# Kernel tuning notes

Hardware: AMD Instinct MI355X
Metric: run time of the kernel (lower is better)

## Reference

```python
import jax, jax.numpy as jnp
import numpy as np

NH = 8          # attention heads
TOP_K = 2       # MoE top-k


def _ln(x, g, b, eps=1e-5):
    mu = x.mean(-1, keepdims=True)
    var = ((x - mu) ** 2).mean(-1, keepdims=True)
    return (x - mu) * jax.lax.rsqrt(var + eps) * g + b


def setup_inputs() -> dict:
    key = jax.random.key(0)
    ks = jax.random.split(key, 12)
    B, C, S, P, E, HID, NEXP, NCLS = 128, 3, 224, 16, 256, 1024, 6, 1000
    N = (S // P) ** 2
    def n(k, shape, scale=0.02):
        return scale * jax.random.normal(k, shape, jnp.float32)
    return dict(
        x=jax.random.normal(ks[0], (B, C, S, S), jnp.float32),
        conv_w=n(ks[1], (E, C, P, P)),
        conv_b=jnp.zeros((E,), jnp.float32),
        pos_embed=n(ks[2], (1, N, E)),
        ln1_g=jnp.ones((E,), jnp.float32), ln1_b=jnp.zeros((E,), jnp.float32),
        wqkv=n(ks[3], (3 * E, E)), bqkv=jnp.zeros((3 * E,), jnp.float32),
        wo=n(ks[4], (E, E)), bo=jnp.zeros((E,), jnp.float32),
        router_w=n(ks[5], (NEXP, E)), router_b=jnp.zeros((NEXP,), jnp.float32),
        w1=n(ks[6], (NEXP, E, HID)), b1=jnp.zeros((NEXP, HID), jnp.float32),
        w2=n(ks[7], (NEXP, HID, E)), b2=jnp.zeros((NEXP, E), jnp.float32),
        ln2_g=jnp.ones((E,), jnp.float32), ln2_b=jnp.zeros((E,), jnp.float32),
        head_w=n(ks[8], (NCLS, E)), head_b=jnp.zeros((NCLS,), jnp.float32),
    )


def reference(x, conv_w, conv_b, pos_embed, ln1_g, ln1_b, wqkv, bqkv, wo, bo,
              router_w, router_b, w1, b1, w2, b2, ln2_g, ln2_b, head_w, head_b):
    B, C, S, _ = x.shape
    E, _, P, _ = conv_w.shape
    G = S // P
    N = G * G
    hd = E // NH
    # --- patch embedding: strided conv == per-patch linear ---
    xr = x.reshape(B, C, G, P, G, P)
    tok = jnp.einsum('bchpwq,ecpq->bhwe', xr, conv_w).reshape(B, N, E) + conv_b
    tok = tok + pos_embed  # dropout is identity in eval
    # --- self-attention block (pre-norm, residual) ---
    xn = _ln(tok, ln1_g, ln1_b)
    qkv = xn @ wqkv.T + bqkv
    q, k, v = jnp.split(qkv, 3, axis=-1)
    q = q.reshape(B, N, NH, hd)
    k = k.reshape(B, N, NH, hd)
    v = v.reshape(B, N, NH, hd)
    scores = jnp.einsum('bqhd,bkhd->bhqk', q, k) / np.float32(np.sqrt(hd))
    attn = jax.nn.softmax(scores, axis=-1)
    ao = jnp.einsum('bhqk,bkhd->bqhd', attn, v).reshape(B, N, E)
    x1 = tok + ao @ wo.T + bo
    # --- MoE (top-k routing, eval: no noise) ---
    T = B * N
    flat = x1.reshape(T, E)
    probs = jax.nn.softmax(flat @ router_w.T + router_b, axis=-1)
    topw, topi = jax.lax.top_k(probs, TOP_K)  # [T,k]
    out = jnp.zeros_like(flat)
    n_experts = router_w.shape[0]
    for e in range(n_experts):  # fixed small expert loop
        gate = jnp.sum(jnp.where(topi == e, topw, 0.0), axis=-1)  # [T], 0 if unrouted
        h = jax.nn.gelu(flat @ w1[e] + b1[e], approximate=False)
        y = h @ w2[e] + b2[e]
        out = out + gate[:, None] * y
    # --- final norm, pool, head ---
    x2 = _ln(out.reshape(B, N, E), ln2_g, ln2_b)
    pooled = x2.mean(axis=1)
    return pooled @ head_w.T + head_b
```

## Files before the change

### kernel.cpp

```cpp
#include <hip/hip_runtime.h>
#include <hip/hip_bf16.h>

typedef unsigned short u16;
typedef short short8 __attribute__((ext_vector_type(8)));
typedef float f32x4 __attribute__((ext_vector_type(4)));

#define T_TOK 25088
#define NTOK 196
#define SWZ(r, c) ((((((c) >> 3) ^ ((r) & 7)) << 3)) | ((c) & 7))

__device__ __forceinline__ u16 bfbits(float v) {
  __hip_bfloat16 h = __float2bfloat16(v);
  return *reinterpret_cast<u16*>(&h);
}
__device__ __forceinline__ float b2f(u16 u) {
  __hip_bfloat16 h = *reinterpret_cast<__hip_bfloat16*>(&u);
  return __bfloat162float(h);
}
__device__ __forceinline__ void fsplit(float v, u16& hi, u16& lo) {
  hi = bfbits(v);
  lo = bfbits(v - b2f(hi));
}

template<int EPI, bool SPLITA>
__global__ __launch_bounds__(256) void gemm_bs(
    const u16* __restrict__ A, const u16* __restrict__ Al,
    const u16* __restrict__ Bh, const u16* __restrict__ Bl,
    int M, int N, int K,
    const float* __restrict__ bias, const float* __restrict__ extra,
    float* __restrict__ outf, u16* __restrict__ obh)
{
  __shared__ u16 As[128][40];
  __shared__ u16 Asl[SPLITA ? 128 : 1][40];
  __shared__ u16 Bsh[128][40], Bsl[128][40];
  const int tid = threadIdx.x;
  const int lane = tid & 63, wave = tid >> 6;
  const int wm = wave >> 1, wn = wave & 1;
  const int row0 = blockIdx.x * 128, col0 = blockIdx.y * 128;

  const int r0 = tid >> 2, r1 = r0 + 64, co = (tid & 3) * 8;
  const int ar0 = row0 + r0, ar1 = row0 + r1;

  f32x4 acc[4][4];
  const f32x4 zero = {0.f, 0.f, 0.f, 0.f};
#pragma unroll
  for (int i = 0; i < 4; ++i)
#pragma unroll
    for (int j = 0; j < 4; ++j) acc[i][j] = zero;

  const int rsel = lane & 15, ksel = (lane >> 4) * 8;

  short8 ra0, ra1, rl0, rl1, rb0, rb1, rc0, rc1;
  auto issue = [&](int k0) {
    ra0 = *(const short8*)(A + (size_t)ar0 * K + k0 + co);
    ra1 = *(const short8*)(A + (size_t)ar1 * K + k0 + co);
    if constexpr (SPLITA) {
      rl0 = *(const short8*)(Al + (size_t)ar0 * K + k0 + co);
      rl1 = *(const short8*)(Al + (size_t)ar1 * K + k0 + co);
    }
    rb0 = *(const short8*)(Bh + (size_t)(col0 + r0) * K + k0 + co);
    rb1 = *(const short8*)(Bh + (size_t)(col0 + r1) * K + k0 + co);
    rc0 = *(const short8*)(Bl + (size_t)(col0 + r0) * K + k0 + co);
    rc1 = *(const short8*)(Bl + (size_t)(col0 + r1) * K + k0 + co);
  };
  auto commit = [&]() {
    *(short8*)&As[r0][co] = ra0;
    *(short8*)&As[r1][co] = ra1;
    if constexpr (SPLITA) {
      *(short8*)&Asl[r0][co] = rl0;
      *(short8*)&Asl[r1][co] = rl1;
    }
    *(short8*)&Bsh[r0][co] = rb0;
    *(short8*)&Bsh[r1][co] = rb1;
    *(short8*)&Bsl[r0][co] = rc0;
    *(short8*)&Bsl[r1][co] = rc1;
  };

  issue(0);
  commit();
  __syncthreads();

  for (int k0 = 0;;) {
    const bool more = (k0 + 32 < K);
    if (more) issue(k0 + 32);
    short8 af[4], al4[4], bh4[4], bl4[4];
#pragma unroll
    for (int i = 0; i < 4; ++i) {
      af[i] = *(const short8*)&As[wm * 64 + i * 16 + rsel][ksel];
      if constexpr (SPLITA) al4[i] = *(const short8*)&Asl[wm * 64 + i * 16 + rsel][ksel];
    }
#pragma unroll
    for (int j = 0; j < 4; ++j) {
      bh4[j] = *(const short8*)&Bsh[wn * 64 + j * 16 + rsel][ksel];
      bl4[j] = *(const short8*)&Bsl[wn * 64 + j * 16 + rsel][ksel];
    }
#pragma unroll
    for (int i = 0; i < 4; ++i)
#pragma unroll
      for (int j = 0; j < 4; ++j) {
        acc[i][j] = __builtin_amdgcn_mfma_f32_16x16x32_bf16(af[i], bh4[j], acc[i][j], 0, 0, 0);
        if constexpr (SPLITA)
          acc[i][j] = __builtin_amdgcn_mfma_f32_16x16x32_bf16(al4[i], bh4[j], acc[i][j], 0, 0, 0);
        acc[i][j] = __builtin_amdgcn_mfma_f32_16x16x32_bf16(af[i], bl4[j], acc[i][j], 0, 0, 0);
      }
    k0 += 32;
    if (!more) break;
    __syncthreads();
    commit();
    __syncthreads();
  }

#pragma unroll
  for (int i = 0; i < 4; ++i) {
#pragma unroll
    for (int j = 0; j < 4; ++j) {
#pragma unroll
      for (int r = 0; r < 4; ++r) {
        int grow = row0 + wm * 64 + i * 16 + (lane >> 4) * 4 + r;
        int gcol = col0 + wn * 64 + j * 16 + (lane & 15);
        float v = acc[i][j][r] + bias[gcol];
        size_t oi = (size_t)grow * N + gcol;
        if constexpr (EPI == 1) {
          v += extra[(size_t)(grow % NTOK) * N + gcol];
          outf[oi] = v;
        } else if constexpr (EPI == 2) {
          v += extra[oi];
          outf[oi] = v;
          obh[oi] = bfbits(v);
        } else if constexpr (EPI == 5) {
          obh[oi] = bfbits(v);
        }
      }
    }
  }
}

__global__ __launch_bounds__(512, 4) void moe_fused(
    const u16* __restrict__ x1h,
    const u16* __restrict__ w1, const u16* __restrict__ w2,
    const float* __restrict__ b1, const float* __restrict__ b2,
    const float* __restrict__ gates,
    const int* __restrict__ idx_all, const int* __restrict__ cnt_all,
    const int* __restrict__ base_all,
    float* __restrict__ yslot)
{
  const int e = blockIdx.z;
  const int Meff = cnt_all[e];
  const int row0 = blockIdx.x * 64;
  if (row0 >= Meff) return;
  const int* gidx = idx_all + (size_t)e * T_TOK;
  const int hbase = base_all[e];
  const u16* W1 = w1 + (size_t)e * 262144;
  const u16* W2 = w2 + (size_t)e * 262144;
  const float* B1 = b1 + e * 1024;
  const float* B2 = b2 + e * 256;

  __shared__ u16 Xs[64][256];
  __shared__ u16 Hs[64][128];
  __shared__ u16 Ws[2 * 128 * 64];

  const int tid = threadIdx.x, lane = tid & 63, wave = tid >> 6;
  const int wm = wave >> 2, wn = wave & 3;
  const int rsel = lane & 15, ksel = (lane >> 4) * 8;
  const f32x4 zero = {0.f, 0.f, 0.f, 0.f};

  const int w1r = tid >> 2, w1c = ((2 * tid) & 7) * 8;
  const int w2r = tid >> 1, w2c = ((4 * tid) & 7) * 8;

  short8 w1a = *(const short8*)(W1 + (size_t)w1r * 256 + w1c);
  short8 w1b = *(const short8*)(W1 + (size_t)w1r * 256 + w1c + 8);
  for (int ch = tid; ch < 2048; ch += 512) {
    int r = ch >> 5, c = (ch & 31) * 8;
    int ar = gidx[min(row0 + r, Meff - 1)];
    *(short8*)&Xs[r][SWZ(r, c)] = *(const short8*)(x1h + (size_t)ar * 256 + c);
  }

  f32x4 acc2[2][4];
#pragma unroll
  for (int i = 0; i < 2; ++i)
#pragma unroll
    for (int j = 0; j < 4; ++j) acc2[i][j] = zero;

  f32x4 acc1[2][2];

  auto ph1 = [&](int st, int buf) {
#pragma unroll
    for (int kk = 0; kk < 2; ++kk) {
      int ra0 = wm * 32 + rsel, ra1 = ra0 + 16;
      int kc = st * 64 + kk * 32 + ksel;
      short8 a0 = *(const short8*)&Xs[ra0][SWZ(ra0, kc)];
      short8 a1 = *(const short8*)&Xs[ra1][SWZ(ra1, kc)];
      int rb0 = wn * 32 + rsel, rb1 = rb0 + 16;
      int wc = kk * 32 + ksel;
      short8 b0 = *(const short8*)&Ws[buf * 8192 + rb0 * 64 + SWZ(rb0, wc)];
      short8 b1 = *(const short8*)&Ws[buf * 8192 + rb1 * 64 + SWZ(rb1, wc)];
      acc1[0][0] = __builtin_amdgcn_mfma_f32_16x16x32_bf16(a0, b0, acc1[0][0], 0, 0, 0);
      acc1[0][1] = __builtin_amdgcn_mfma_f32_16x16x32_bf16(a0, b1, acc1[0][1], 0, 0, 0);
      acc1[1][0] = __builtin_amdgcn_mfma_f32_16x16x32_bf16(a1, b0, acc1[1][0], 0, 0, 0);
      acc1[1][1] = __builtin_amdgcn_mfma_f32_16x16x32_bf16(a1, b1, acc1[1][1], 0, 0, 0);
    }
  };
  auto ph2 = [&](int st) {
#pragma unroll
    for (int kk = 0; kk < 2; ++kk) {
      int ra0 = wm * 32 + rsel, ra1 = ra0 + 16;
      int kc = st * 64 + kk * 32 + ksel;
      short8 a0 = *(const short8*)&Hs[ra0][SWZ(ra0, kc)];
      short8 a1 = *(const short8*)&Hs[ra1][SWZ(ra1, kc)];
      int wc = kk * 32 + ksel;
#pragma unroll
      for (int nj = 0; nj < 4; ++nj) {
        int nr = wn * 64 + nj * 16 + rsel;
        short8 b = *(const short8*)&Ws[nr * 64 + SWZ(nr, wc)];
        acc2[0][nj] = __builtin_amdgcn_mfma_f32_16x16x32_bf16(a0, b, acc2[0][nj], 0, 0, 0);
        acc2[1][nj] = __builtin_amdgcn_mfma_f32_16x16x32_bf16(a1, b, acc2[1][nj], 0, 0, 0);
      }
    }
  };

  for (int hc = 0; hc < 8; ++hc) {
    const u16* W1c = W1 + (size_t)hc * 128 * 256;
    const u16* W2c = W2 + hc * 128;
    short8 q0 = *(const short8*)(W2c + (size_t)w2r * 1024 + w2c);
    short8 q1 = *(const short8*)(W2c + (size_t)w2r * 1024 + w2c + 8);
    short8 q2 = *(const short8*)(W2c + (size_t)w2r * 1024 + w2c + 16);
    short8 q3 = *(const short8*)(W2c + (size_t)w2r * 1024 + w2c + 24);

#pragma unroll
    for (int i = 0; i < 2; ++i) {
      acc1[i][0] = zero; acc1[i][1] = zero;
    }

    *(short8*)&Ws[w1r * 64 + SWZ(w1r, w1c)] = w1a;
    *(short8*)&Ws[w1r * 64 + SWZ(w1r, w1c + 8)] = w1b;
    short8 p0 = *(const short8*)(W1c + (size_t)w1r * 256 + 64 + w1c);
    short8 p1 = *(const short8*)(W1c + (size_t)w1r * 256 + 64 + w1c + 8);
    __syncthreads();
    short8 r0 = *(const short8*)(W1c + (size_t)w1r * 256 + 128 + w1c);
    short8 r1 = *(const short8*)(W1c + (size_t)w1r * 256 + 128 + w1c + 8);
    ph1(0, 0);
    *(short8*)&Ws[8192 + w1r * 64 + SWZ(w1r, w1c)] = p0;
    *(short8*)&Ws[8192 + w1r * 64 + SWZ(w1r, w1c + 8)] = p1;
    __syncthreads();
    p0 = *(const short8*)(W1c + (size_t)w1r * 256 + 192 + w1c);
    p1 = *(const short8*)(W1c + (size_t)w1r * 256 + 192 + w1c + 8);
    ph1(1, 1);
    *(short8*)&Ws[w1r * 64 + SWZ(w1r, w1c)] = r0;
    *(short8*)&Ws[w1r * 64 + SWZ(w1r, w1c + 8)] = r1;
    __syncthreads();
    ph1(2, 0);
    *(short8*)&Ws[8192 + w1r * 64 + SWZ(w1r, w1c)] = p0;
    *(short8*)&Ws[8192 + w1r * 64 + SWZ(w1r, w1c + 8)] = p1;
    __syncthreads();
    ph1(3, 1);

#pragma unroll
    for (int mi = 0; mi < 2; ++mi)
#pragma unroll
      for (int nj = 0; nj < 2; ++nj)
#pragma unroll
        for (int r = 0; r < 4; ++r) {
          int tr = wm * 32 + mi * 16 + (lane >> 4) * 4 + r;
          int tc = wn * 32 + nj * 16 + rsel;
          float v = acc1[mi][nj][r] + B1[hc * 128 + tc];
          float u = 1.5957691216057308f * (v + 0.044715f * v * v * v);
          Hs[tr][SWZ(tr, tc)] = bfbits(v / (1.f + __expf(-u)));
        }
    __syncthreads();

    *(short8*)&Ws[w2r * 64 + SWZ(w2r, w2c)] = q0;
    *(short8*)&Ws[w2r * 64 + SWZ(w2r, w2c + 8)] = q1;
    *(short8*)&Ws[w2r * 64 + SWZ(w2r, w2c + 16)] = q2;
    *(short8*)&Ws[w2r * 64 + SWZ(w2r, w2c + 24)] = q3;
    q0 = *(const short8*)(W2c + (size_t)w2r * 1024 + 64 + w2c);
    q1 = *(const short8*)(W2c + (size_t)w2r * 1024 + 64 + w2c + 8);
    q2 = *(const short8*)(W2c + (size_t)w2r * 1024 + 64 + w2c + 16);
    q3 = *(const short8*)(W2c + (size_t)w2r * 1024 + 64 + w2c + 24);
    __syncthreads();
    ph2(0);
    __syncthreads();
    *(short8*)&Ws[w2r * 64 + SWZ(w2r, w2c)] = q0;
    *(short8*)&Ws[w2r * 64 + SWZ(w2r, w2c + 8)] = q1;
    *(short8*)&Ws[w2r * 64 + SWZ(w2r, w2c + 16)] = q2;
    *(short8*)&Ws[w2r * 64 + SWZ(w2r, w2c + 24)] = q3;
    if (hc < 7) {
      w1a = *(const short8*)(W1 + (size_t)((hc + 1) * 128 + w1r) * 256 + w1c);
      w1b = *(const short8*)(W1 + (size_t)((hc + 1) * 128 + w1r) * 256 + w1c + 8);
    }
    __syncthreads();
    ph2(1);
    __syncthreads();
  }

#pragma unroll
  for (int mi = 0; mi < 2; ++mi)
#pragma unroll
    for (int r = 0; r < 4; ++r) {
      int grow = row0 + wm * 32 + mi * 16 + (lane >> 4) * 4 + r;
      if (grow < Meff) {
        int tk = gidx[grow];
        float gt = gates[(size_t)tk * 6 + e];
#pragma unroll
        for (int nj = 0; nj < 4; ++nj) {
          int gcol = wn * 64 + nj * 16 + rsel;
          yslot[(size_t)(hbase + grow) * 256 + gcol] = gt * (acc2[mi][nj][r] + B2[gcol]);
        }
      }
    }
}

__global__ void im2col_split(const float* __restrict__ x,
                             u16* __restrict__ Aph, u16* __restrict__ Apl) {
  int id = blockIdx.x * 256 + threadIdx.x;
  if (id >= T_TOK * 192) return;
  int t = id / 192, kk = id - t * 192;
  int k4 = kk * 4;
  int c = k4 >> 8, rem = k4 & 255, p = rem >> 4, q = rem & 15;
  int b = t / 196, n = t - b * 196, gh = n / 14, gw = n - gh * 14;
  const float4 v = *(const float4*)(x + ((size_t)(b * 3 + c) * 224 + gh * 16 + p) * 224 + gw * 16 + q);
  u16 h0, l0, h1, l1, h2, l2, h3, l3;
  fsplit(v.x, h0, l0); fsplit(v.y, h1, l1); fsplit(v.z, h2, l2); fsplit(v.w, h3, l3);
  *(ushort4*)(Aph + (size_t)t * 768 + k4) = make_ushort4(h0, h1, h2, h3);
  *(ushort4*)(Apl + (size_t)t * 768 + k4) = make_ushort4(l0, l1, l2, l3);
}

__global__ __launch_bounds__(256) void ln_kernel(const float* __restrict__ in,
    const float* __restrict__ g, const float* __restrict__ b, u16* __restrict__ oh)
{
  const int lane = threadIdx.x & 63;
  const int t = blockIdx.x * 4 + (threadIdx.x >> 6);
  const float4 v = *(const float4*)(in + (size_t)t * 256 + lane * 4);
  float s = v.x + v.y + v.z + v.w;
  float sq = v.x * v.x + v.y * v.y + v.z * v.z + v.w * v.w;
#pragma unroll
  for (int o = 32; o >= 1; o >>= 1) {
    s  += __shfl_xor(s,  o, 64);
    sq += __shfl_xor(sq, o, 64);
  }
  float mu = s * (1.f / 256.f);
  float var = sq * (1.f / 256.f) - mu * mu;
  float rstd = rsqrtf(var + 1e-5f);
  const float4 gv = *(const float4*)(g + lane * 4);
  const float4 bv = *(const float4*)(b + lane * 4);
  *(ushort4*)(oh + (size_t)t * 256 + lane * 4) = make_ushort4(
      bfbits((v.x - mu) * rstd * gv.x + bv.x), bfbits((v.y - mu) * rstd * gv.y + bv.y),
      bfbits((v.z - mu) * rstd * gv.z + bv.z), bfbits((v.w - mu) * rstd * gv.w + bv.w));
}

__global__ __launch_bounds__(256) void ln2_combine(const float* __restrict__ yslot,
    const int* __restrict__ invslot,
    const float* __restrict__ g, const float* __restrict__ b, float* __restrict__ outf)
{
  const int lane = threadIdx.x & 63;
  const int t = blockIdx.x * 4 + (threadIdx.x >> 6);
  const int s0 = invslot[t * 2], s1 = invslot[t * 2 + 1];
  const float4 a = *(const float4*)(yslot + (size_t)s0 * 256 + lane * 4);
  const float4 c = *(const float4*)(yslot + (size_t)s1 * 256 + lane * 4);
  float4 v = make_float4(a.x + c.x, a.y + c.y, a.z + c.z, a.w + c.w);
  float s = v.x + v.y + v.z + v.w;
  float sq = v.x * v.x + v.y * v.y + v.z * v.z + v.w * v.w;
#pragma unroll
  for (int o = 32; o >= 1; o >>= 1) {
    s  += __shfl_xor(s,  o, 64);
    sq += __shfl_xor(sq, o, 64);
  }
  float mu = s * (1.f / 256.f);
  float var = sq * (1.f / 256.f) - mu * mu;
  float rstd = rsqrtf(var + 1e-5f);
  const float4 gv = *(const float4*)(g + lane * 4);
  const float4 bv = *(const float4*)(b + lane * 4);
  *(float4*)(outf + (size_t)t * 256 + lane * 4) = make_float4(
      (v.x - mu) * rstd * gv.x + bv.x, (v.y - mu) * rstd * gv.y + bv.y,
      (v.z - mu) * rstd * gv.z + bv.z, (v.w - mu) * rstd * gv.w + bv.w);
}

__global__ __launch_bounds__(256) void attn_mfma(const u16* __restrict__ qkvb,
                                                 u16* __restrict__ aoh, u16* __restrict__ aol) {
  __shared__ u16 Qs[208][40];
  __shared__ u16 Ks[208][40];
  __shared__ u16 Vt[32][256];
  __shared__ u16 Ps[4][16][232];
  const int tid = threadIdx.x, lane = tid & 63, wave = tid >> 6;
  const int b = blockIdx.x >> 3, h = blockIdx.x & 7;
  const size_t base = (size_t)b * 196 * 768 + h * 32;
  const short8 z8 = {0, 0, 0, 0, 0, 0, 0, 0};

  for (int idx = tid; idx < 832; idx += 256) {
    int r = idx >> 2, c = (idx & 3) * 8;
    short8 q = z8, k = z8;
    if (r < 196) {
      q = *(const short8*)(qkvb + base + (size_t)r * 768 + c);
// ... 193 lines not shown
  const int e = blockIdx.z;
  const int bc = blockIdx.x * 32, br = blockIdx.y * 32;
  const int tx = threadIdx.x & 31, ty = threadIdx.x >> 5;
  const float* src = in + (size_t)e * R * C;
#pragma unroll
  for (int i = 0; i < 32; i += 8)
    tile[ty + i][tx] = src[(size_t)(br + ty + i) * C + bc + tx];
  __syncthreads();
#pragma unroll
  for (int i = 0; i < 32; i += 8) {
    size_t di = (size_t)e * R * C + (size_t)(bc + ty + i) * R + br + tx;
    oh[di] = bfbits(tile[tx][ty + i]);
  }
}

extern "C" void kernel_launch(void* const* d_in, const int* in_sizes, int n_in,
                              void* d_out, int out_size, void* d_ws, size_t ws_size,
                              hipStream_t stream) {
  (void)in_sizes; (void)n_in; (void)out_size; (void)ws_size;
  const float* x      = (const float*)d_in[0];
  const float* conv_w = (const float*)d_in[1];
  const float* conv_b = (const float*)d_in[2];
  const float* pos    = (const float*)d_in[3];
  const float* ln1_g  = (const float*)d_in[4];
  const float* ln1_b  = (const float*)d_in[5];
  const float* wqkv   = (const float*)d_in[6];
  const float* bqkv   = (const float*)d_in[7];
  const float* wo     = (const float*)d_in[8];
  const float* bo     = (const float*)d_in[9];
  const float* rw     = (const float*)d_in[10];
  const float* rb     = (const float*)d_in[11];
  const float* w1     = (const float*)d_in[12];
  const float* b1     = (const float*)d_in[13];
  const float* w2     = (const float*)d_in[14];
  const float* b2     = (const float*)d_in[15];
  const float* ln2_g  = (const float*)d_in[16];
  const float* ln2_b  = (const float*)d_in[17];
  const float* hw     = (const float*)d_in[18];
  const float* hb     = (const float*)d_in[19];
  float* out = (float*)d_out;

  const int T = T_TOK;
  char* ws = (char*)d_ws;
  size_t off = 0;
  auto alloc = [&](size_t bytes) -> void* {
    void* p = ws + off;
    off += (bytes + 255) & ~(size_t)255;
    return p;
  };
  u16*   Aph    = (u16*)  alloc((size_t)T * 768 * 2);
  u16*   Apl    = (u16*)  alloc((size_t)T * 768 * 2);
  float* tok    = (float*)alloc((size_t)T * 256 * 4);
  u16*   xnh    = (u16*)  alloc((size_t)T * 256 * 2);
  u16*   qkvb   = (u16*)  alloc((size_t)T * 768 * 2);
  u16*   aoh    = (u16*)  alloc((size_t)T * 256 * 2);
  u16*   aol    = (u16*)  alloc((size_t)T * 256 * 2);
  float* x1f    = (float*)alloc((size_t)T * 256 * 4);
  u16*   x1h    = (u16*)  alloc((size_t)T * 256 * 2);
  float* gates  = (float*)alloc((size_t)T * 6 * 4);
  int*   idx    = (int*)  alloc((size_t)6 * T * 4);
  int*   cnt    = (int*)  alloc(256);
  int*   base   = (int*)  alloc(256);
  int*   nslot  = (int*)  alloc((size_t)T * 4);
  int*   invslot= (int*)  alloc((size_t)2 * T * 4);
  float* pooled = (float*)alloc((size_t)128 * 256 * 4);
  u16*   cwh    = (u16*)  alloc((size_t)196608 * 2);
  u16*   cwl    = (u16*)  alloc((size_t)196608 * 2);
  u16*   wqh    = (u16*)  alloc((size_t)196608 * 2);
  u16*   wql    = (u16*)  alloc((size_t)196608 * 2);
  u16*   woh    = (u16*)  alloc((size_t)65536 * 2);
  u16*   wol    = (u16*)  alloc((size_t)65536 * 2);
  u16*   w1th   = (u16*)  alloc((size_t)6 * 262144 * 2);
  u16*   w2th   = (u16*)  alloc((size_t)6 * 262144 * 2);
  float* yslot = (float*)aoh;
  float* x2    = (float*)ws;

  cast_split_kernel<<<192, 256, 0, stream>>>(conv_w, cwh, cwl, 49152);
  cast_split_kernel<<<192, 256, 0, stream>>>(wqkv, wqh, wql, 49152);
  cast_split_kernel<<<64, 256, 0, stream>>>(wo, woh, wol, 16384);
  transpose_cast<<<dim3(32, 8, 6), 256, 0, stream>>>(w1, w1th, 256, 1024);
  transpose_cast<<<dim3(8, 32, 6), 256, 0, stream>>>(w2, w2th, 1024, 256);

  im2col_split<<<18816, 256, 0, stream>>>(x, Aph, Apl);
  gemm_bs<1, true><<<dim3(196, 2), 256, 0, stream>>>(Aph, Apl, cwh, cwl, T, 256, 768,
      conv_b, pos, tok, nullptr);

  ln_kernel<<<6272, 256, 0, stream>>>(tok, ln1_g, ln1_b, xnh);
  gemm_bs<5, false><<<dim3(196, 6), 256, 0, stream>>>(xnh, nullptr, wqh, wql, T, 768, 256,
      bqkv, nullptr, nullptr, qkvb);
  attn_mfma<<<1024, 256, 0, stream>>>(qkvb, aoh, aol);
  gemm_bs<2, true><<<dim3(196, 2), 256, 0, stream>>>(aoh, aol, woh, wol, T, 256, 256,
      bo, tok, x1f, x1h);

  router_kernel<<<6272, 256, 0, stream>>>(x1f, rw, rb, gates);
  hipMemsetAsync(cnt, 0, 256, stream);
  scatter_kernel<<<98, 256, 0, stream>>>(gates, cnt, idx);
  prefix6_kernel<<<1, 64, 0, stream>>>(cnt, base);
  hipMemsetAsync(nslot, 0, (size_t)T * 4, stream);
  slotmap_kernel<<<dim3(98, 6), 256, 0, stream>>>(idx, cnt, base, nslot, invslot);
  moe_fused<<<dim3(392, 1, 6), 512, 0, stream>>>(x1h, w1th, w2th,
      b1, b2, gates, idx, cnt, base, yslot);

  ln2_combine<<<6272, 256, 0, stream>>>(yslot, invslot, ln2_g, ln2_b, x2);
  pool_kernel<<<128, 256, 0, stream>>>(x2, pooled);
  head_kernel<<<128, 256, 0, stream>>>(pooled, hw, hb, out);
}
```

Measured before the change: 429.2 us.

## Load GEMM B operands directly from global into registers and shrink tiles

Measured after the change: 471.7 us. +9.9%, slower.

```diff
diff --git a/kernel.cpp b/kernel.cpp
--- a/kernel.cpp
+++ b/kernel.cpp
@@ -23,101 +23,94 @@
 }
 
 template<int EPI, bool SPLITA>
-__global__ __launch_bounds__(256) void gemm_bs(
+__global__ __launch_bounds__(256, 4) void gemm_bs(
     const u16* __restrict__ A, const u16* __restrict__ Al,
     const u16* __restrict__ Bh, const u16* __restrict__ Bl,
     int M, int N, int K,
     const float* __restrict__ bias, const float* __restrict__ extra,
     float* __restrict__ outf, u16* __restrict__ obh)
 {
-  __shared__ u16 As[128][40];
-  __shared__ u16 Asl[SPLITA ? 128 : 1][40];
-  __shared__ u16 Bsh[128][40], Bsl[128][40];
+  __shared__ u16 As[2][64][40];
+  __shared__ u16 Asl[SPLITA ? 2 : 1][64][40];
   const int tid = threadIdx.x;
-  const int lane = tid & 63, wave = tid >> 6;
-  const int wm = wave >> 1, wn = wave & 1;
-  const int row0 = blockIdx.x * 128, col0 = blockIdx.y * 128;
-
-  const int r0 = tid >> 2, r1 = r0 + 64, co = (tid & 3) * 8;
-  const int ar0 = row0 + r0, ar1 = row0 + r1;
-
-  f32x4 acc[4][4];
+  const int lane = tid & 63, wn = tid >> 6;
+  const int row0 = blockIdx.x * 64, col0 = blockIdx.y * 128;
+  const int rsel = lane & 15, ksel = (lane >> 4) * 8;
+
+  const int sr = tid >> 2, sc = (tid & 3) * 8;
+  const int ar = row0 + sr;
+
+  const u16* bph0 = Bh + (size_t)(col0 + wn * 32 + rsel) * K;
+  const u16* bph1 = Bh + (size_t)(col0 + wn * 32 + 16 + rsel) * K;
+  const u16* bpl0 = Bl + (size_t)(col0 + wn * 32 + rsel) * K;
+  const u16* bpl1 = Bl + (size_t)(col0 + wn * 32 + 16 + rsel) * K;
+
+  f32x4 acc[4][2];
   const f32x4 zero = {0.f, 0.f, 0.f, 0.f};
 #pragma unroll
-  for (int i = 0; i < 4; ++i)
-#pragma unroll
-    for (int j = 0; j < 4; ++j) acc[i][j] = zero;
-
-  const int rsel = lane & 15, ksel = (lane >> 4) * 8;
-
-  short8 ra0, ra1, rl0, rl1, rb0, rb1, rc0, rc1;
-  auto issue = [&](int k0) {
-    ra0 = *(const short8*)(A + (size_t)ar0 * K + k0 + co);
-    ra1 = *(const short8*)(A + (size_t)ar1 * K + k0 + co);
-    if constexpr (SPLITA) {
-      rl0 = *(const short8*)(Al + (size_t)ar0 * K + k0 + co);
-      rl1 = *(const short8*)(Al + (size_t)ar1 * K + k0 + co);
-    }
-    rb0 = *(const short8*)(Bh + (size_t)(col0 + r0) * K + k0 + co);
-    rb1 = *(const short8*)(Bh + (size_t)(col0 + r1) * K + k0 + co);
-    rc0 = *(const short8*)(Bl + (size_t)(col0 + r0) * K + k0 + co);
-    rc1 = *(const short8*)(Bl + (size_t)(col0 + r1) * K + k0 + co);
+  for (int i = 0; i < 4; ++i) { acc[i][0] = zero; acc[i][1] = zero; }
+
+  short8 ra, rl;
+  auto issueA = [&](int k0) {
+    ra = *(const short8*)(A + (size_t)ar * K + k0 + sc);
+    if constexpr (SPLITA) rl = *(const short8*)(Al + (size_t)ar * K + k0 + sc);
   };
-  auto commit = [&]() {
-    *(short8*)&As[r0][co] = ra0;
-    *(short8*)&As[r1][co] = ra1;
-    if constexpr (SPLITA) {
-      *(short8*)&Asl[r0][co] = rl0;
-      *(short8*)&Asl[r1][co] = rl1;
-    }
-    *(short8*)&Bsh[r0][co] = rb0;
-    *(short8*)&Bsh[r1][co] = rb1;
-    *(short8*)&Bsl[r0][co] = rc0;
-    *(short8*)&Bsl[r1][co] = rc1;
+  auto commitA = [&](int buf) {
+    *(short8*)&As[buf][sr][sc] = ra;
+    if constexpr (SPLITA) *(short8*)&Asl[buf][sr][sc] = rl;
   };
 
-  issue(0);
-  commit();
-  __syncthreads();
-
+  issueA(0);
+  commitA(0);
+  short8 b0 = *(const short8*)(bph0 + ksel);
+  short8 b1 = *(const short8*)(bph1 + ksel);
+  short8 c0 = *(const short8*)(bpl0 + ksel);
+  short8 c1 = *(const short8*)(bpl1 + ksel);
+  __syncthreads();
+
+  int buf = 0;
   for (int k0 = 0;;) {
     const bool more = (k0 + 32 < K);
-    if (more) issue(k0 + 32);
-    short8 af[4], al4[4], bh4[4], bl4[4];
+    if (more) issueA(k0 + 32);
+    short8 ub0 = b0, ub1 = b1, uc0 = c0, uc1 = c1;
+    if (more) {
+      b0 = *(const short8*)(bph0 + k0 + 32 + ksel);
+      b1 = *(const short8*)(bph1 + k0 + 32 + ksel);
+      c0 = *(const short8*)(bpl0 + k0 + 32 + ksel);
+      c1 = *(const short8*)(bpl1 + k0 + 32 + ksel);
+    }
+    short8 af[4], alf[4];
 #pragma unroll
     for (int i = 0; i < 4; ++i) {
-      af[i] = *(const short8*)&As[wm * 64 + i * 16 + rsel][ksel];
-      if constexpr (SPLITA) al4[i] = *(const short8*)&Asl[wm * 64 + i * 16 + rsel][ksel];
-    }
-#pragma unroll
-    for (int j = 0; j < 4; ++j) {
-      bh4[j] = *(const short8*)&Bsh[wn * 64 + j * 16 + rsel][ksel];
-      bl4[j] = *(const short8*)&Bsl[wn * 64 + j * 16 + rsel][ksel];
-    }
-#pragma unroll
-    for (int i = 0; i < 4; ++i)
-#pragma unroll
-      for (int j = 0; j < 4; ++j) {
-        acc[i][j] = __builtin_amdgcn_mfma_f32_16x16x32_bf16(af[i], bh4[j], acc[i][j], 0, 0, 0);
-        if constexpr (SPLITA)
-          acc[i][j] = __builtin_amdgcn_mfma_f32_16x16x32_bf16(al4[i], bh4[j], acc[i][j], 0, 0, 0);
-        acc[i][j] = __builtin_amdgcn_mfma_f32_16x16x32_bf16(af[i], bl4[j], acc[i][j], 0, 0, 0);
-      }
+      af[i] = *(const short8*)&As[buf][i * 16 + rsel][ksel];
+      if constexpr (SPLITA) alf[i] = *(const short8*)&Asl[buf][i * 16 + rsel][ksel];
+    }
+#pragma unroll
+    for (int i = 0; i < 4; ++i) {
+      acc[i][0] = __builtin_amdgcn_mfma_f32_16x16x32_bf16(af[i], ub0, acc[i][0], 0, 0, 0);
+      acc[i][1] = __builtin_amdgcn_mfma_f32_16x16x32_bf16(af[i], ub1, acc[i][1], 0, 0, 0);
+      if constexpr (SPLITA) {
+        acc[i][0] = __builtin_amdgcn_mfma_f32_16x16x32_bf16(alf[i], ub0, acc[i][0], 0, 0, 0);
+        acc[i][1] = __builtin_amdgcn_mfma_f32_16x16x32_bf16(alf[i], ub1, acc[i][1], 0, 0, 0);
+      }
+      acc[i][0] = __builtin_amdgcn_mfma_f32_16x16x32_bf16(af[i], uc0, acc[i][0], 0, 0, 0);
+      acc[i][1] = __builtin_amdgcn_mfma_f32_16x16x32_bf16(af[i], uc1, acc[i][1], 0, 0, 0);
+    }
     k0 += 32;
     if (!more) break;
+    commitA(buf ^ 1);
     __syncthreads();
-    commit();
-    __syncthreads();
+    buf ^= 1;
   }
 
 #pragma unroll
   for (int i = 0; i < 4; ++i) {
 #pragma unroll
-    for (int j = 0; j < 4; ++j) {
+    for (int j = 0; j < 2; ++j) {
 #pragma unroll
       for (int r = 0; r < 4; ++r) {
-        int grow = row0 + wm * 64 + i * 16 + (lane >> 4) * 4 + r;
-        int gcol = col0 + wn * 64 + j * 16 + (lane & 15);
+        int grow = row0 + i * 16 + (lane >> 4) * 4 + r;
+        int gcol = col0 + wn * 32 + j * 16 + rsel;
         float v = acc[i][j][r] + bias[gcol];
         size_t oi = (size_t)grow * N + gcol;
         if constexpr (EPI == 1) {
@@ -157,152 +150,91 @@
 
   __shared__ u16 Xs[64][256];
   __shared__ u16 Hs[64][128];
-  __shared__ u16 Ws[2 * 128 * 64];
-
-  const int tid = threadIdx.x, lane = tid & 63, wave = tid >> 6;
-  const int wm = wave >> 2, wn = wave & 3;
+
+  const int tid = threadIdx.x, lane = tid & 63, wn = tid >> 6;
   const int rsel = lane & 15, ksel = (lane >> 4) * 8;
   const f32x4 zero = {0.f, 0.f, 0.f, 0.f};
 
-  const int w1r = tid >> 2, w1c = ((2 * tid) & 7) * 8;
-  const int w2r = tid >> 1, w2c = ((4 * tid) & 7) * 8;
-
-  short8 w1a = *(const short8*)(W1 + (size_t)w1r * 256 + w1c);
-  short8 w1b = *(const short8*)(W1 + (size_t)w1r * 256 + w1c + 8);
   for (int ch = tid; ch < 2048; ch += 512) {
     int r = ch >> 5, c = (ch & 31) * 8;
-    int ar = gidx[min(row0 + r, Meff - 1)];
-    *(short8*)&Xs[r][SWZ(r, c)] = *(const short8*)(x1h + (size_t)ar * 256 + c);
-  }
-
-  f32x4 acc2[2][4];
-#pragma unroll
-  for (int i = 0; i < 2; ++i)
-#pragma unroll
-    for (int j = 0; j < 4; ++j) acc2[i][j] = zero;
-
-  f32x4 acc1[2][2];
-
-  auto ph1 = [&](int st, int buf) {
-#pragma unroll
-    for (int kk = 0; kk < 2; ++kk) {
-      int ra0 = wm * 32 + rsel, ra1 = ra0 + 16;
-      int kc = st * 64 + kk * 32 + ksel;
-      short8 a0 = *(const short8*)&Xs[ra0][SWZ(ra0, kc)];
-      short8 a1 = *(const short8*)&Xs[ra1][SWZ(ra1, kc)];
-      int rb0 = wn * 32 + rsel, rb1 = rb0 + 16;
-      int wc = kk * 32 + ksel;
-      short8 b0 = *(const short8*)&Ws[buf * 8192 + rb0 * 64 + SWZ(rb0, wc)];
-      short8 b1 = *(const short8*)&Ws[buf * 8192 + rb1 * 64 + SWZ(rb1, wc)];
-      acc1[0][0] = __builtin_amdgcn_mfma_f32_16x16x32_bf16(a0, b0, acc1[0][0], 0, 0, 0);
-      acc1[0][1] = __builtin_amdgcn_mfma_f32_16x16x32_bf16(a0, b1, acc1[0][1], 0, 0, 0);
-      acc1[1][0] = __builtin_amdgcn_mfma_f32_16x16x32_bf16(a1, b0, acc1[1][0], 0, 0, 0);
-      acc1[1][1] = __builtin_amdgcn_mfma_f32_16x16x32_bf16(a1, b1, acc1[1][1], 0, 0, 0);
-    }
-  };
-  auto ph2 = [&](int st) {
-#pragma unroll
-    for (int kk = 0; kk < 2; ++kk) {
-      int ra0 = wm * 32 + rsel, ra1 = ra0 + 16;
-      int kc = st * 64 + kk * 32 + ksel;
-      short8 a0 = *(const short8*)&Hs[ra0][SWZ(ra0, kc)];
-      short8 a1 = *(const short8*)&Hs[ra1][SWZ(ra1, kc)];
-      int wc = kk * 32 + ksel;
-#pragma unroll
-      for (int nj = 0; nj < 4; ++nj) {
-        int nr = wn * 64 + nj * 16 + rsel;
-        short8 b = *(const short8*)&Ws[nr * 64 + SWZ(nr, wc)];
-        acc2[0][nj] = __builtin_amdgcn_mfma_f32_16x16x32_bf16(a0, b, acc2[0][nj], 0, 0, 0);
-        acc2[1][nj] = __builtin_amdgcn_mfma_f32_16x16x32_bf16(a1, b, acc2[1][nj], 0, 0, 0);
-      }
-    }
-  };
+    int arr = gidx[min(row0 + r, Meff - 1)];
+    *(short8*)&Xs[r][SWZ(r, c)] = *(const short8*)(x1h + (size_t)arr * 256 + c);
+  }
+  __syncthreads();
+
+  f32x4 acc2[4][2];
+#pragma unroll
+  for (int i = 0; i < 4; ++i) { acc2[i][0] = zero; acc2[i][1] = zero; }
+
+  const u16* w1p  = W1 + (size_t)(wn * 16 + rsel) * 256;
+  const u16* w2p0 = W2 + (size_t)(wn * 32 + rsel) * 1024;
+  const u16* w2p1 = W2 + (size_t)(wn * 32 + 16 + rsel) * 1024;
 
   for (int hc = 0; hc < 8; ++hc) {
-    const u16* W1c = W1 + (size_t)hc * 128 * 256;
-    const u16* W2c = W2 + hc * 128;
-    short8 q0 = *(const short8*)(W2c + (size_t)w2r * 1024 + w2c);
-    short8 q1 = *(const short8*)(W2c + (size_t)w2r * 1024 + w2c + 8);
-    short8 q2 = *(const short8*)(W2c + (size_t)w2r * 1024 + w2c + 16);
-    short8 q3 = *(const short8*)(W2c + (size_t)w2r * 1024 + w2c + 24);
-
-#pragma unroll
-    for (int i = 0; i < 2; ++i) {
-      acc1[i][0] = zero; acc1[i][1] = zero;
-    }
-
-    *(short8*)&Ws[w1r * 64 + SWZ(w1r, w1c)] = w1a;
-    *(short8*)&Ws[w1r * 64 + SWZ(w1r, w1c + 8)] = w1b;
-    short8 p0 = *(const short8*)(W1c + (size_t)w1r * 256 + 64 + w1c);
-    short8 p1 = *(const short8*)(W1c + (size_t)w1r * 256 + 64 + w1c + 8);
+    const u16* w1c = w1p + (size_t)hc * 128 * 256;
+
+    f32x4 acc1[4];
+#pragma unroll
+    for (int i = 0; i < 4; ++i) acc1[i] = zero;
+
+    short8 pb = *(const short8*)(w1c + ksel);
+#pragma unroll
+    for (int kk = 0; kk < 8; ++kk) {
+      short8 ub = pb;
+      if (kk < 7) pb = *(const short8*)(w1c + (kk + 1) * 32 + ksel);
+      int kc = kk * 32 + ksel;
+#pragma unroll
+      for (int mi = 0; mi < 4; ++mi) {
+        int rr = mi * 16 + rsel;
+        short8 a = *(const short8*)&Xs[rr][SWZ(rr, kc)];
+        acc1[mi] = __builtin_amdgcn_mfma_f32_16x16x32_bf16(a, ub, acc1[mi], 0, 0, 0);
+      }
+    }
+
+#pragma unroll
+    for (int mi = 0; mi < 4; ++mi)
+#pragma unroll
+      for (int r = 0; r < 4; ++r) {
+        int tr = mi * 16 + (lane >> 4) * 4 + r;
+        int tc = wn * 16 + rsel;
+        float v = acc1[mi][r] + B1[hc * 128 + tc];
+        float u = 1.5957691216057308f * (v + 0.044715f * v * v * v);
+        Hs[tr][SWZ(tr, tc)] = bfbits(v / (1.f + __expf(-u)));
+      }
     __syncthreads();
-    short8 r0 = *(const short8*)(W1c + (size_t)w1r * 256 + 128 + w1c);
-    short8 r1 = *(const short8*)(W1c + (size_t)w1r * 256 + 128 + w1c + 8);
-    ph1(0, 0);
-    *(short8*)&Ws[8192 + w1r * 64 + SWZ(w1r, w1c)] = p0;
-    *(short8*)&Ws[8192 + w1r * 64 + SWZ(w1r, w1c + 8)] = p1;
+
+    short8 q0 = *(const short8*)(w2p0 + hc * 128 + ksel);
+    short8 q1 = *(const short8*)(w2p1 + hc * 128 + ksel);
+#pragma unroll
+    for (int kk = 0; kk < 4; ++kk) {
+      short8 u0 = q0, u1 = q1;
+      if (kk < 3) {
+        q0 = *(const short8*)(w2p0 + hc * 128 + (kk + 1) * 32 + ksel);
+        q1 = *(const short8*)(w2p1 + hc * 128 + (kk + 1) * 32 + ksel);
+      }
+      int kc = kk * 32 + ksel;
+#pragma unroll
+      for (int mi = 0; mi < 4; ++mi) {
+        int rr = mi * 16 + rsel;
+        short8 a = *(const short8*)&Hs[rr][SWZ(rr, kc)];
+        acc2[mi][0] = __builtin_amdgcn_mfma_f32_16x16x32_bf16(a, u0, acc2[mi][0], 0, 0, 0);
+        acc2[mi][1] = __builtin_amdgcn_mfma_f32_16x16x32_bf16(a, u1, acc2[mi][1], 0, 0, 0);
+      }
+    }
     __syncthreads();
-    p0 = *(const short8*)(W1c + (size_t)w1r * 256 + 192 + w1c);
-    p1 = *(const short8*)(W1c + (size_t)w1r * 256 + 192 + w1c + 8);
-    ph1(1, 1);
-    *(short8*)&Ws[w1r * 64 + SWZ(w1r, w1c)] = r0;
-    *(short8*)&Ws[w1r * 64 + SWZ(w1r, w1c + 8)] = r1;
-    __syncthreads();
-    ph1(2, 0);
-    *(short8*)&Ws[8192 + w1r * 64 + SWZ(w1r, w1c)] = p0;
-    *(short8*)&Ws[8192 + w1r * 64 + SWZ(w1r, w1c + 8)] = p1;
-    __syncthreads();
-    ph1(3, 1);
-
-#pragma unroll
-    for (int mi = 0; mi < 2; ++mi)
-#pragma unroll
-      for (int nj = 0; nj < 2; ++nj)
-#pragma unroll
-        for (int r = 0; r < 4; ++r) {
-          int tr = wm * 32 + mi * 16 + (lane >> 4) * 4 + r;
-          int tc = wn * 32 + nj * 16 + rsel;
-          float v = acc1[mi][nj][r] + B1[hc * 128 + tc];
-          float u = 1.5957691216057308f * (v + 0.044715f * v * v * v);
-          Hs[tr][SWZ(tr, tc)] = bfbits(v / (1.f + __expf(-u)));
-        }
-    __syncthreads();
-
-    *(short8*)&Ws[w2r * 64 + SWZ(w2r, w2c)] = q0;
-    *(short8*)&Ws[w2r * 64 + SWZ(w2r, w2c + 8)] = q1;
-    *(short8*)&Ws[w2r * 64 + SWZ(w2r, w2c + 16)] = q2;
-    *(short8*)&Ws[w2r * 64 + SWZ(w2r, w2c + 24)] = q3;
-    q0 = *(const short8*)(W2c + (size_t)w2r * 1024 + 64 + w2c);
-    q1 = *(const short8*)(W2c + (size_t)w2r * 1024 + 64 + w2c + 8);
-    q2 = *(const short8*)(W2c + (size_t)w2r * 1024 + 64 + w2c + 16);
-    q3 = *(const short8*)(W2c + (size_t)w2r * 1024 + 64 + w2c + 24);
-    __syncthreads();
-    ph2(0);
-    __syncthreads();
-    *(short8*)&Ws[w2r * 64 + SWZ(w2r, w2c)] = q0;
-    *(short8*)&Ws[w2r * 64 + SWZ(w2r, w2c + 8)] = q1;
-    *(short8*)&Ws[w2r * 64 + SWZ(w2r, w2c + 16)] = q2;
-    *(short8*)&Ws[w2r * 64 + SWZ(w2r, w2c + 24)] = q3;
-    if (hc < 7) {
-      w1a = *(const short8*)(W1 + (size_t)((hc + 1) * 128 + w1r) * 256 + w1c);
-      w1b = *(const short8*)(W1 + (size_t)((hc + 1) * 128 + w1r) * 256 + w1c + 8);
-    }
-    __syncthreads();
-    ph2(1);
-    __syncthreads();
-  }
-
-#pragma unroll
-  for (int mi = 0; mi < 2; ++mi)
+  }
+
+#pragma unroll
+  for (int mi = 0; mi < 4; ++mi)
 #pragma unroll
     for (int r = 0; r < 4; ++r) {
-      int grow = row0 + wm * 32 + mi * 16 + (lane >> 4) * 4 + r;
+      int grow = row0 + mi * 16 + (lane >> 4) * 4 + r;
       if (grow < Meff) {
         int tk = gidx[grow];
         float gt = gates[(size_t)tk * 6 + e];
 #pragma unroll
-        for (int nj = 0; nj < 4; ++nj) {
-          int gcol = wn * 64 + nj * 16 + rsel;
+        for (int nj = 0; nj < 2; ++nj) {
+          int gcol = wn * 32 + nj * 16 + rsel;
           yslot[(size_t)(hbase + grow) * 256 + gcol] = gt * (acc2[mi][nj][r] + B2[gcol]);
         }
       }
@@ -666,14 +598,14 @@
   transpose_cast<<<dim3(8, 32, 6), 256, 0, stream>>>(w2, w2th, 1024, 256);
 
   im2col_split<<<18816, 256, 0, stream>>>(x, Aph, Apl);
-  gemm_bs<1, true><<<dim3(196, 2), 256, 0, stream>>>(Aph, Apl, cwh, cwl, T, 256, 768,
+  gemm_bs<1, true><<<dim3(392, 2), 256, 0, stream>>>(Aph, Apl, cwh, cwl, T, 256, 768,
       conv_b, pos, tok, nullptr);
 
   ln_kernel<<<6272, 256, 0, stream>>>(tok, ln1_g, ln1_b, xnh);
-  gemm_bs<5, false><<<dim3(196, 6), 256, 0, stream>>>(xnh, nullptr, wqh, wql, T, 768, 256,
+  gemm_bs<5, false><<<dim3(392, 6), 256, 0, stream>>>(xnh, nullptr, wqh, wql, T, 768, 256,
       bqkv, nullptr, nullptr, qkvb);
   attn_mfma<<<1024, 256, 0, stream>>>(qkvb, aoh, aol);
-  gemm_bs<2, true><<<dim3(196, 2), 256, 0, stream>>>(aoh, aol, woh, wol, T, 256, 256,
+  gemm_bs<2, true><<<dim3(392, 2), 256, 0, stream>>>(aoh, aol, woh, wol, T, 256, 256,
       bo, tok, x1f, x1h);
 
   router_kernel<<<6272, 256, 0, stream>>>(x1f, rw, rb, gates);
```

## Transpose MoE expert GEMM tiling so waves own weight rows and vectorize outputs

Applied to the files above, without the earlier changes.

After: 421.8 us. Within noise of the previous version (-1.7%).

```diff
diff --git a/kernel.cpp b/kernel.cpp
--- a/kernel.cpp
+++ b/kernel.cpp
@@ -3,11 +3,13 @@
 
 typedef unsigned short u16;
 typedef short short8 __attribute__((ext_vector_type(8)));
+typedef short short4v __attribute__((ext_vector_type(4)));
 typedef float f32x4 __attribute__((ext_vector_type(4)));
 
 #define T_TOK 25088
 #define NTOK 196
 #define SWZ(r, c) ((((((c) >> 3) ^ ((r) & 7)) << 3)) | ((c) & 7))
+#define SWZ4(r, c) ((((((c) >> 2) & 16) | ((((c) >> 2) ^ (r)) & 15)) << 2) | ((c) & 3))
 
 __device__ __forceinline__ u16 bfbits(float v) {
   __hip_bfloat16 h = __float2bfloat16(v);
@@ -50,25 +52,28 @@
 
   const int rsel = lane & 15, ksel = (lane >> 4) * 8;
 
-  short8 ra0, ra1, rl0, rl1, rb0, rb1, rc0, rc1;
+  short8 ra, rl, rb0, rb1, rc0, rc1;
   auto issue = [&](int k0) {
-    ra0 = *(const short8*)(A + (size_t)ar0 * K + k0 + co);
-    ra1 = *(const short8*)(A + (size_t)ar1 * K + k0 + co);
-    if constexpr (SPLITA) {
-      rl0 = *(const short8*)(Al + (size_t)ar0 * K + k0 + co);
-      rl1 = *(const short8*)(Al + (size_t)ar1 * K + k0 + co);
-    }
+    ra = *(const short8*)(A + (size_t)ar0 * K + k0 + co);
+    rl = *(const short8*)(A + (size_t)ar1 * K + k0 + co);
     rb0 = *(const short8*)(Bh + (size_t)(col0 + r0) * K + k0 + co);
     rb1 = *(const short8*)(Bh + (size_t)(col0 + r1) * K + k0 + co);
     rc0 = *(const short8*)(Bl + (size_t)(col0 + r0) * K + k0 + co);
     rc1 = *(const short8*)(Bl + (size_t)(col0 + r1) * K + k0 + co);
   };
+  short8 sa, sl;
+  auto issueS = [&](int k0) {
+    if constexpr (SPLITA) {
+      sa = *(const short8*)(Al + (size_t)ar0 * K + k0 + co);
+      sl = *(const short8*)(Al + (size_t)ar1 * K + k0 + co);
+    }
+  };
   auto commit = [&]() {
-    *(short8*)&As[r0][co] = ra0;
-    *(short8*)&As[r1][co] = ra1;
+    *(short8*)&As[r0][co] = ra;
+    *(short8*)&As[r1][co] = rl;
     if constexpr (SPLITA) {
-      *(short8*)&Asl[r0][co] = rl0;
-      *(short8*)&Asl[r1][co] = rl1;
+      *(short8*)&Asl[r0][co] = sa;
+      *(short8*)&Asl[r1][co] = sl;
     }
     *(short8*)&Bsh[r0][co] = rb0;
     *(short8*)&Bsh[r1][co] = rb1;
@@ -77,12 +82,13 @@
   };
 
   issue(0);
+  issueS(0);
   commit();
   __syncthreads();
 
   for (int k0 = 0;;) {
     const bool more = (k0 + 32 < K);
-    if (more) issue(k0 + 32);
+    if (more) { issue(k0 + 32); issueS(k0 + 32); }
     short8 af[4], al4[4], bh4[4], bl4[4];
 #pragma unroll
     for (int i = 0; i < 4; ++i) {
@@ -117,7 +123,7 @@
 #pragma unroll
       for (int r = 0; r < 4; ++r) {
         int grow = row0 + wm * 64 + i * 16 + (lane >> 4) * 4 + r;
-        int gcol = col0 + wn * 64 + j * 16 + (lane & 15);
+        int gcol = col0 + wn * 64 + j * 16 + rsel;
         float v = acc[i][j][r] + bias[gcol];
         size_t oi = (size_t)grow * N + gcol;
         if constexpr (EPI == 1) {
@@ -159,8 +165,7 @@
   __shared__ u16 Hs[64][128];
   __shared__ u16 Ws[2 * 128 * 64];
 
-  const int tid = threadIdx.x, lane = tid & 63, wave = tid >> 6;
-  const int wm = wave >> 2, wn = wave & 3;
+  const int tid = threadIdx.x, lane = tid & 63, wn = tid >> 6;
   const int rsel = lane & 15, ksel = (lane >> 4) * 8;
   const f32x4 zero = {0.f, 0.f, 0.f, 0.f};
 
@@ -171,8 +176,8 @@
   short8 w1b = *(const short8*)(W1 + (size_t)w1r * 256 + w1c + 8);
   for (int ch = tid; ch < 2048; ch += 512) {
     int r = ch >> 5, c = (ch & 31) * 8;
-    int ar = gidx[min(row0 + r, Meff - 1)];
-    *(short8*)&Xs[r][SWZ(r, c)] = *(const short8*)(x1h + (size_t)ar * 256 + c);
+    int arr = gidx[min(row0 + r, Meff - 1)];
+    *(short8*)&Xs[r][SWZ(r, c)] = *(const short8*)(x1h + (size_t)arr * 256 + c);
   }
 
   f32x4 acc2[2][4];
@@ -181,39 +186,43 @@
 #pragma unroll
     for (int j = 0; j < 4; ++j) acc2[i][j] = zero;
 
-  f32x4 acc1[2][2];
+  f32x4 acc1[4];
 
   auto ph1 = [&](int st, int buf) {
 #pragma unroll
     for (int kk = 0; kk < 2; ++kk) {
-      int ra0 = wm * 32 + rsel, ra1 = ra0 + 16;
-      int kc = st * 64 + kk * 32 + ksel;
-      short8 a0 = *(const short8*)&Xs[ra0][SWZ(ra0, kc)];
-      short8 a1 = *(const short8*)&Xs[ra1][SWZ(ra1, kc)];
-      int rb0 = wn * 32 + rsel, rb1 = rb0 + 16;
+      int wrow = wn * 16 + rsel;
       int wc = kk * 32 + ksel;
-      short8 b0 = *(const short8*)&Ws[buf * 8192 + rb0 * 64 + SWZ(rb0, wc)];
-      short8 b1 = *(const short8*)&Ws[buf * 8192 + rb1 * 64 + SWZ(rb1, wc)];
-      acc1[0][0] = __builtin_amdgcn_mfma_f32_16x16x32_bf16(a0, b0, acc1[0][0], 0, 0, 0);
-      acc1[0][1] = __builtin_amdgcn_mfma_f32_16x16x32_bf16(a0, b1, acc1[0][1], 0, 0, 0);
-      acc1[1][0] = __builtin_amdgcn_mfma_f32_16x16x32_bf16(a1, b0, acc1[1][0], 0, 0, 0);
-      acc1[1][1] = __builtin_amdgcn_mfma_f32_16x16x32_bf16(a1, b1, acc1[1][1], 0, 0, 0);
+      short8 wf = *(const short8*)&Ws[buf * 8192 + wrow * 64 + SWZ(wrow, wc)];
+      int kglob = st * 64 + kk * 32 + ksel;
+#pragma unroll
+      for (int tt = 0; tt < 4; ++tt) {
+        int xrow = tt * 16 + rsel;
+        short8 xf = *(const short8*)&Xs[xrow][SWZ(xrow, kglob)];
+        acc1[tt] = __builtin_amdgcn_mfma_f32_16x16x32_bf16(wf, xf, acc1[tt], 0, 0, 0);
+      }
     }
   };
   auto ph2 = [&](int st) {
 #pragma unroll
     for (int kk = 0; kk < 2; ++kk) {
-      int ra0 = wm * 32 + rsel, ra1 = ra0 + 16;
+      int wc = kk * 32 + ksel;
+      short8 wf[2];
+#pragma unroll
+      for (int ot = 0; ot < 2; ++ot) {
+        int wrow = wn * 32 + ot * 16 + rsel;
+        wf[ot] = *(const short8*)&Ws[wrow * 64 + SWZ(wrow, wc)];
+      }
       int kc = st * 64 + kk * 32 + ksel;
-      short8 a0 = *(const short8*)&Hs[ra0][SWZ(ra0, kc)];
-      short8 a1 = *(const short8*)&Hs[ra1][SWZ(ra1, kc)];
-      int wc = kk * 32 + ksel;
-#pragma unroll
-      for (int nj = 0; nj < 4; ++nj) {
-        int nr = wn * 64 + nj * 16 + rsel;
-        short8 b = *(const short8*)&Ws[nr * 64 + SWZ(nr, wc)];
-        acc2[0][nj] = __builtin_amdgcn_mfma_f32_16x16x32_bf16(a0, b, acc2[0][nj], 0, 0, 0);
-        acc2[1][nj] = __builtin_amdgcn_mfma_f32_16x16x32_bf16(a1, b, acc2[1][nj], 0, 0, 0);
+#pragma unroll
+      for (int tt = 0; tt < 4; ++tt) {
+        int tok = tt * 16 + rsel;
+        short4v lo = *(const short4v*)&Hs[tok][SWZ4(tok, kc)];
+        short4v hi = *(const short4v*)&Hs[tok][SWZ4(tok, kc + 4)];
+        short8 hf = {lo[0], lo[1], lo[2], lo[3], hi[0], hi[1], hi[2], hi[3]};
+#pragma unroll
+        for (int ot = 0; ot < 2; ++ot)
+          acc2[ot][tt] = __builtin_amdgcn_mfma_f32_16x16x32_bf16(wf[ot], hf, acc2[ot][tt], 0, 0, 0);
       }
     }
   };
@@ -227,17 +236,15 @@
     short8 q3 = *(const short8*)(W2c + (size_t)w2r * 1024 + w2c + 24);
 
 #pragma unroll
-    for (int i = 0; i < 2; ++i) {
-      acc1[i][0] = zero; acc1[i][1] = zero;
-    }
+    for (int i = 0; i < 4; ++i) acc1[i] = zero;
 
     *(short8*)&Ws[w1r * 64 + SWZ(w1r, w1c)] = w1a;
     *(short8*)&Ws[w1r * 64 + SWZ(w1r, w1c + 8)] = w1b;
     short8 p0 = *(const short8*)(W1c + (size_t)w1r * 256 + 64 + w1c);
     short8 p1 = *(const short8*)(W1c + (size_t)w1r * 256 + 64 + w1c + 8);
     __syncthreads();
-    short8 r0 = *(const short8*)(W1c + (size_t)w1r * 256 + 128 + w1c);
-    short8 r1 = *(const short8*)(W1c + (size_t)w1r * 256 + 128 + w1c + 8);
+    short8 s0 = *(const short8*)(W1c + (size_t)w1r * 256 + 128 + w1c);
+    short8 s1 = *(const short8*)(W1c + (size_t)w1r * 256 + 128 + w1c + 8);
     ph1(0, 0);
     *(short8*)&Ws[8192 + w1r * 64 + SWZ(w1r, w1c)] = p0;
     *(short8*)&Ws[8192 + w1r * 64 + SWZ(w1r, w1c + 8)] = p1;
@@ -245,8 +252,8 @@
     p0 = *(const short8*)(W1c + (size_t)w1r * 256 + 192 + w1c);
     p1 = *(const short8*)(W1c + (size_t)w1r * 256 + 192 + w1c + 8);
     ph1(1, 1);
-    *(short8*)&Ws[w1r * 64 + SWZ(w1r, w1c)] = r0;
-    *(short8*)&Ws[w1r * 64 + SWZ(w1r, w1c + 8)] = r1;
+    *(short8*)&Ws[w1r * 64 + SWZ(w1r, w1c)] = s0;
+    *(short8*)&Ws[w1r * 64 + SWZ(w1r, w1c + 8)] = s1;
     __syncthreads();
     ph1(2, 0);
     *(short8*)&Ws[8192 + w1r * 64 + SWZ(w1r, w1c)] = p0;
@@ -255,17 +262,18 @@
     ph1(3, 1);
 
 #pragma unroll
-    for (int mi = 0; mi < 2; ++mi)
-#pragma unroll
-      for (int nj = 0; nj < 2; ++nj)
-#pragma unroll
-        for (int r = 0; r < 4; ++r) {
-          int tr = wm * 32 + mi * 16 + (lane >> 4) * 4 + r;
-          int tc = wn * 32 + nj * 16 + rsel;
-          float v = acc1[mi][nj][r] + B1[hc * 128 + tc];
-          float u = 1.5957691216057308f * (v + 0.044715f * v * v * v);
-          Hs[tr][SWZ(tr, tc)] = bfbits(v / (1.f + __expf(-u)));
-        }
+    for (int tt = 0; tt < 4; ++tt) {
+      int tok = tt * 16 + rsel;
+      int hid0 = wn * 16 + (lane >> 4) * 4;
+      u16 hv[4];
+#pragma unroll
+      for (int r = 0; r < 4; ++r) {
+        float v = acc1[tt][r] + B1[hc * 128 + hid0 + r];
+        float u = 1.5957691216057308f * (v + 0.044715f * v * v * v);
+        hv[r] = bfbits(v / (1.f + __expf(-u)));
+      }
+      *(ushort4*)&Hs[tok][SWZ4(tok, hid0)] = make_ushort4(hv[0], hv[1], hv[2], hv[3]);
+    }
     __syncthreads();
 
     *(short8*)&Ws[w2r * 64 + SWZ(w2r, w2c)] = q0;
@@ -293,20 +301,22 @@
   }
 
 #pragma unroll
-  for (int mi = 0; mi < 2; ++mi)
-#pragma unroll
-    for (int r = 0; r < 4; ++r) {
-      int grow = row0 + wm * 32 + mi * 16 + (lane >> 4) * 4 + r;
-      if (grow < Meff) {
-        int tk = gidx[grow];
-        float gt = gates[(size_t)tk * 6 + e];
-#pragma unroll
-        for (int nj = 0; nj < 4; ++nj) {
-          int gcol = wn * 64 + nj * 16 + rsel;
-          yslot[(size_t)(hbase + grow) * 256 + gcol] = gt * (acc2[mi][nj][r] + B2[gcol]);
-        }
-      }
-    }
+  for (int tt = 0; tt < 4; ++tt) {
+    int grow = row0 + tt * 16 + rsel;
+    if (grow < Meff) {
+      int tk = gidx[grow];
+      float gt = gates[(size_t)tk * 6 + e];
+#pragma unroll
+      for (int ot = 0; ot < 2; ++ot) {
+        int out0 = wn * 32 + ot * 16 + (lane >> 4) * 4;
+        float4 w4 = make_float4(gt * (acc2[ot][tt][0] + B2[out0]),
+                                gt * (acc2[ot][tt][1] + B2[out0 + 1]),
+                                gt * (acc2[ot][tt][2] + B2[out0 + 2]),
+                                gt * (acc2[ot][tt][3] + B2[out0 + 3]));
+        *(float4*)&yslot[(size_t)(hbase + grow) * 256 + out0] = w4;
+      }
+    }
+  }
 }
 
 __global__ void im2col_split(const float* __restrict__ x,
```
